# Performance work log

Hardware: AMD Instinct MI355X
Metric: run time of the kernel (lower is better)

Reference implementation:

```python
import jax, jax.numpy as jnp
import numpy as np

N_QUBITS = 12
R = 1
EDGES = [(i, (i + 1) % N_QUBITS) for i in range(N_QUBITS)]
DIM = 2 ** N_QUBITS
BATCH = 64
_LET = 'abcdefghijklmnopqrstuvwxy'

_I4 = np.eye(4, dtype=np.float32)
_AD = np.fliplr(_I4).copy()                      # antidiagonal (XX imag pattern)
_YP = np.array([[0,0,0,1],[0,0,-1,0],[0,-1,0,0],[1,0,0,0]], dtype=np.float32)  # YY imag pattern
_CNOT = jnp.asarray(np.array([[1,0,0,0],[0,1,0,0],[0,0,0,1],[0,0,1,0]], dtype=np.complex64))
_k = np.arange(DIM)
# z_signs[i, k] = -1 if bit (n-i-1) of k is set, matching the torch buffer
_ZS = jnp.asarray(np.stack([1.0 - 2.0 * ((_k >> (N_QUBITS - i - 1)) & 1) for i in range(N_QUBITS)]).astype(np.float32))  # [n, 2^n]


def _c(r, i):
    return jax.lax.complex(r, i)


def rx_mat(t):
    c, s, z = jnp.cos(t / 2), jnp.sin(t / 2), jnp.zeros_like(t)
    real = jnp.stack([jnp.stack([c, z], -1), jnp.stack([z, c], -1)], -2)
    imag = jnp.stack([jnp.stack([z, -s], -1), jnp.stack([-s, z], -1)], -2)
    return _c(real, imag)


def ry_mat(t):
    c, s = jnp.cos(t / 2), jnp.sin(t / 2)
    real = jnp.stack([jnp.stack([c, -s], -1), jnp.stack([s, c], -1)], -2)
    return _c(real, jnp.zeros_like(real))


def rz_mat(t):
    p, z = t / 2, jnp.zeros_like(t)
    cp, sp = jnp.cos(p), jnp.sin(p)
    real = jnp.stack([jnp.stack([cp, z], -1), jnp.stack([z, cp], -1)], -2)
    imag = jnp.stack([jnp.stack([-sp, z], -1), jnp.stack([z, sp], -1)], -2)
    return _c(real, imag)


def ising_zz(t):
    p = t / 2
    c, s = jnp.cos(p), jnp.sin(p)
    dr = jnp.stack([c, c, c, c], -1)
    di = jnp.stack([-s, s, s, -s], -1)
    i4 = jnp.asarray(_I4)
    return _c(dr[..., :, None] * i4, di[..., :, None] * i4)


def ising_xx(t):
    c, s = jnp.cos(t / 2), jnp.sin(t / 2)
    return _c(c[..., None, None] * jnp.asarray(_I4), -s[..., None, None] * jnp.asarray(_AD))


def ising_yy(t):
    c, s = jnp.cos(t / 2), jnp.sin(t / 2)
    return _c(c[..., None, None] * jnp.asarray(_I4), s[..., None, None] * jnp.asarray(_YP))


def apply_1q(state, gate, q):
    # state [B, 2^n]; gate [2,2] or [B,2,2]; qubit axis sits at stride 2^q (matches torch view)
    B = state.shape[0]
    left, right = 2 ** (N_QUBITS - q - 1), 2 ** q
    s = state.reshape(B, left, 2, right)
    sub = 'bij' if gate.ndim == 3 else 'ij'
    return jnp.einsum(f'{sub},bljr->blir', gate, s).reshape(B, DIM)


def apply_2q(state, gate, q1, q2):
    # state [B, 2^n]; gate [4,4]; qubit index = tensor-axis index from MSB (matches torch permute path)
    if q1 > q2:
        q1, q2 = q2, q1
    B = state.shape[0]
    s = state.reshape((B,) + (2,) * N_QUBITS)
    g = gate.reshape(2, 2, 2, 2)
    ax = list(_LET[:N_QUBITS])
    out = ax.copy()
    u, v = ax[q1], ax[q2]
    out[q1], out[q2] = 'A', 'B'
    spec = f"AB{u}{v},Z{''.join(ax)}->Z{''.join(out)}"
    return jnp.einsum(spec, g, s).reshape(B, DIM)


def _forward(data, encoding_scale, encoding_bias, eta, ew_zz, ew_xx, ew_yy, nb_z, nb_x, nb_y, trainable_rots):
    B, n = data.shape
    # data-encoding gates, cached once per forward: angles [B, n] -> gates [B, n, 2, 2]
    rx_g = rx_mat(encoding_scale[:, 0] * data + encoding_bias[:, 0])
    ry_g = ry_mat(encoding_scale[:, 1] * data + encoding_bias[:, 1])
    rz_g = rz_mat(encoding_scale[:, 2] * data + encoding_bias[:, 2])
    state = jnp.zeros((B, DIM), jnp.complex64).at[:, 0].set(1.0)
    ising_fns = (ising_zz, ising_xx, ising_yy)
    ews = (ew_zz, ew_xx, ew_yy)
    nbs = (nb_z, nb_x, nb_y)
    bias_fns = (rz_mat, rx_mat, ry_mat)
    enc_types = ('full', 'xy', 'yz')
    for r in range(R):
        for b in range(3):  # blocks: ZZ, XX, YY
            bt = enc_types[b]
            # data encoding
            for q in range(n):
                if bt != 'yz':
                    state = apply_1q(state, rx_g[:, q], q)
                state = apply_1q(state, ry_g[:, q], q)
                if bt != 'xy':
                    state = apply_1q(state, rz_g[:, q], q)
            # Ising interaction on each edge
            theta = eta[r, b] * ews[b][r]            # [n_edges]
            egs = ising_fns[b](theta)                # [n_edges, 4, 4]
            for e, (i, j) in enumerate(EDGES):
                state = apply_2q(state, egs[e], i, j)
            # node biases (RZ / RX / RY matching the block)
            bgs = bias_fns[b](nbs[b][r])             # [n, 2, 2]
            for q in range(n):
                state = apply_1q(state, bgs[q], q)
            # trainable rotations rx, ry, rz per qubit
            rots = trainable_rots[r, b]              # [n, 3]
            rxg, ryg, rzg = rx_mat(rots[:, 0]), ry_mat(rots[:, 1]), rz_mat(rots[:, 2])
            for q in range(n):
                state = apply_1q(state, rxg[q], q)
                state = apply_1q(state, ryg[q], q)
                state = apply_1q(state, rzg[q], q)
            # CNOT entangling ring
            for q in range(n):
                state = apply_2q(state, _CNOT, q, (q + 1) % n)
    probs = state.real ** 2 + state.imag ** 2        # [B, 2^n]
    return probs @ _ZS.T                             # Pauli-Z expectations [B, n]


def setup_inputs() -> dict:
    key = jax.random.key(0)
    ks = jax.random.split(key, 12)
    n, E, f = N_QUBITS, len(EDGES), jnp.float32
    return {
        'data': jax.random.uniform(ks[0], (BATCH, n), f),
        'encoding_scale': jnp.pi * jnp.ones((n, 3), f) + 0.1 * jax.random.normal(ks[1], (n, 3), f),
        'encoding_bias': 0.1 * jax.random.normal(ks[2], (n, 3), f),
        'eta': 0.5 * jnp.ones((R, 3), f),
        'ew_zz': jnp.ones((R, E), f) + 0.1 * jax.random.normal(ks[3], (R, E), f),
        'ew_xx': jnp.ones((R, E), f) + 0.1 * jax.random.normal(ks[4], (R, E), f),
        'ew_yy': jnp.ones((R, E), f) + 0.1 * jax.random.normal(ks[5], (R, E), f),
        'nb_z': 0.1 * jax.random.normal(ks[6], (R, n), f),
        'nb_x': 0.1 * jax.random.normal(ks[7], (R, n), f),
        'nb_y': 0.1 * jax.random.normal(ks[8], (R, n), f),
        'trainable_rots': 0.1 * jax.random.normal(ks[9], (R, 3, n, 3), f),
    }


def reference(data, encoding_scale, encoding_bias, eta, ew_zz, ew_xx, ew_yy, nb_z, nb_x, nb_y, trainable_rots):
    return _forward(data, encoding_scale, encoding_bias, eta, ew_zz, ew_xx, ew_yy, nb_z, nb_x, nb_y, trainable_rots)
```

## Files before the change

kernel.cpp:

```cpp
#include <hip/hip_runtime.h>
#include <math.h>

#define NT 512
#define QDIM 4096

typedef float v2f __attribute__((ext_vector_type(2)));
using F2 = float2;

__device__ __forceinline__ v2f mkv(float x, float y) { v2f r; r.x = x; r.y = y; return r; }

__device__ __forceinline__ v2f cfma(v2f m, v2f a, v2f acc) {
    v2f r;
    asm("v_pk_fma_f32 %0, %1, %2, %3 op_sel:[0,0,0] op_sel_hi:[0,1,1]\n\t"
        "v_pk_fma_f32 %0, %1, %2, %0 op_sel:[1,1,0] op_sel_hi:[1,0,1] neg_lo:[1,0,0]"
        : "=&v"(r) : "v"(m), "v"(a), "v"(acc));
    return r;
}
__device__ __forceinline__ v2f cmulp(v2f m, v2f a) {
    v2f r;
    asm("v_pk_mul_f32 %0, %1, %2 op_sel:[0,0] op_sel_hi:[0,1]\n\t"
        "v_pk_fma_f32 %0, %1, %2, %0 op_sel:[1,1,0] op_sel_hi:[1,0,1] neg_lo:[1,0,0]"
        : "=&v"(r) : "v"(m), "v"(a));
    return r;
}

__device__ __forceinline__ F2 cadd(F2 p, F2 q) { return make_float2(p.x + q.x, p.y + q.y); }
__device__ __forceinline__ F2 cmul(F2 p, F2 q) {
    return make_float2(p.x * q.x - p.y * q.y, p.x * q.y + p.y * q.x);
}
struct M2 { F2 a, b, c, d; };
__device__ __forceinline__ M2 mmul(M2 A, M2 B) {
    M2 R;
    R.a = cadd(cmul(A.a, B.a), cmul(A.b, B.c));
    R.b = cadd(cmul(A.a, B.b), cmul(A.b, B.d));
    R.c = cadd(cmul(A.c, B.a), cmul(A.d, B.c));
    R.d = cadd(cmul(A.c, B.b), cmul(A.d, B.d));
    return R;
}
__device__ __forceinline__ M2 mrx(float t) {
    float s, c; sincosf(0.5f * t, &s, &c);
    return { make_float2(c, 0), make_float2(0, -s), make_float2(0, -s), make_float2(c, 0) };
}
__device__ __forceinline__ M2 mry(float t) {
    float s, c; sincosf(0.5f * t, &s, &c);
    return { make_float2(c, 0), make_float2(-s, 0), make_float2(s, 0), make_float2(c, 0) };
}
__device__ __forceinline__ M2 mrz(float t) {
    float s, c; sincosf(0.5f * t, &s, &c);
    return { make_float2(c, -s), make_float2(0, 0), make_float2(0, 0), make_float2(c, s) };
}
#define RSQ2 0.70710678118654752f
__device__ __forceinline__ M2 mH() {
    return { make_float2(RSQ2, 0), make_float2(RSQ2, 0), make_float2(RSQ2, 0), make_float2(-RSQ2, 0) };
}
__device__ __forceinline__ M2 mW() {
    return { make_float2(RSQ2, 0), make_float2(0, RSQ2), make_float2(RSQ2, 0), make_float2(0, -RSQ2) };
}
__device__ __forceinline__ M2 mWd() {
    return { make_float2(RSQ2, 0), make_float2(RSQ2, 0), make_float2(0, -RSQ2), make_float2(0, RSQ2) };
}


template<int Li>
__device__ __forceinline__ int kOf(int t, int j) {
    const int mlo = (1 << (3 * Li)) - 1;
    return (t & mlo) | (j << (3 * Li)) | ((t & ~mlo) << 3);
}
__device__ __forceinline__ int slot0(int k) {
    int j = k & 7, t = k >> 3;
    return j * 512 + (t ^ j);
}

template<int TYPE>
__device__ __forceinline__ void itrip(v2f* amp, int l, v2f* wb) {
#pragma unroll
    for (int j = 0; j < 8; ++j) wb[j * 64 + (l ^ ((9 * j) & 63))] = amp[j];
    asm volatile("" ::: "memory");
#pragma unroll
    for (int j = 0; j < 8; ++j) {
        int jo, lo;
        if (TYPE == 0) { jo = l & 7;        lo = j | (l & 56); }
        else           { jo = (l >> 3) & 7; lo = (l & 7) | (j << 3); }
        amp[j] = wb[jo * 64 + (lo ^ ((9 * jo) & 63))];
    }
}

__device__ __forceinline__ void btrip(v2f* amp, int tid, int l, int wv, v2f* b) {
#pragma unroll
    for (int j = 0; j < 8; ++j) b[j * 512 + (tid ^ j)] = amp[j];
    __syncthreads();
#pragma unroll
    for (int j = 0; j < 8; ++j) amp[j] = b[wv * 512 + ((j * 64 + l) ^ wv)];
}

struct Trio { v2f m[12]; };

__device__ __forceinline__ Trio load_trio(const float4 (*g4)[2]) {
    Trio t;
#pragma unroll
    for (int k = 0; k < 3; ++k) {
        float4 a = g4[k][0], b = g4[k][1];
        t.m[k * 4 + 0] = mkv(a.x, a.y); t.m[k * 4 + 1] = mkv(a.z, a.w);
        t.m[k * 4 + 2] = mkv(b.x, b.y); t.m[k * 4 + 3] = mkv(b.z, b.w);
    }
    return t;
}

template<int JB>
__device__ __forceinline__ void g1_reg(v2f* amp, const v2f* g) {
    const int m = 1 << JB;
    v2f m00 = g[0], m01 = g[1], m10 = g[2], m11 = g[3];
#pragma unroll
    for (int j = 0; j < 8; ++j)
        if (!(j & m)) {
            v2f a = amp[j], b = amp[j | m];
            amp[j]     = cfma(m01, b, cmulp(m00, a));
            amp[j | m] = cfma(m11, b, cmulp(m10, a));
        }
}
__device__ __forceinline__ void apply_trio(v2f* amp, const Trio& t) {
    g1_reg<0>(amp, t.m + 0);  g1_reg<1>(amp, t.m + 4);  g1_reg<2>(amp, t.m + 8);
}

__device__ __forceinline__ void diag_L3(v2f* amp, const float* zh, int tid) {
    float phi0 = 0.f;
#pragma unroll
    for (int e = 3; e <= 10; ++e) {
        int hi = 11 - e, lo = 10 - e;
        phi0 += (((tid >> hi) ^ (tid >> lo)) & 1) ? zh[e] : -zh[e];
    }
    float z0 = zh[0], z1 = zh[1], z2 = zh[2], z11 = zh[11];
    int t8 = (tid >> 8) & 1, t0 = tid & 1;
#pragma unroll
    for (int j = 0; j < 8; ++j) {
        int j0 = j & 1, j1 = (j >> 1) & 1, j2 = (j >> 2) & 1;
        float phi = phi0
            + ((j2 ^ j1) ? z0 : -z0)
            + ((j1 ^ j0) ? z1 : -z1)
            + ((j0 ^ t8) ? z2 : -z2)
            + ((j2 ^ t0) ? z11 : -z11);
        float sp, cp;
        __sincosf(phi, &sp, &cp);
        amp[j] = cmulp(mkv(cp, sp), amp[j]);
    }
}

__device__ __forceinline__ int cnot_src(int k) {
#pragma unroll
    for (int e = 11; e >= 0; --e) {
        int hi = (e < 11) ? 11 - e : 11, lo = (e < 11) ? 10 - e : 0;
        if ((k >> hi) & 1) k ^= (1 << lo);
    }
    return k;
}

__device__ __forceinline__ void cnot_trip(v2f* amp, int tid, const int* kslot, v2f* b) {
#pragma unroll
    for (int j = 0; j < 8; ++j) b[j * 512 + (tid ^ j)] = amp[j];
    __syncthreads();
#pragma unroll
    for (int j = 0; j < 8; ++j) amp[j] = b[kslot[j]];
}

__global__ __launch_bounds__(NT) void qsim_kernel(
    const float* __restrict__ data,
    const float* __restrict__ enc_scale,
    const float* __restrict__ enc_bias,
    const float* __restrict__ eta,
    const float* __restrict__ ew_zz,
    const float* __restrict__ ew_xx,
    const float* __restrict__ ew_yy,
    const float* __restrict__ nb_z,
    const float* __restrict__ nb_x,
    const float* __restrict__ nb_y,
    const float* __restrict__ trots,
    float* __restrict__ out)
{
    __shared__ v2f bbuf[2][QDIM];
    __shared__ v2f ibuf[QDIM];
    __shared__ float4 g1q4[72][2];
    __shared__ float zhalf[3][12];
    __shared__ float red[8][12];

    const int tid = threadIdx.x;
    const int l = tid & 63, wv = tid >> 6;
    const int bat = blockIdx.x;
    v2f* wb = &ibuf[wv * 512];

    if (tid < 36) {
        int b = tid / 12, q = tid % 12;
        float x  = data[bat * 12 + q];
        float ax = enc_scale[q * 3 + 0] * x + enc_bias[q * 3 + 0];
        float ay = enc_scale[q * 3 + 1] * x + enc_bias[q * 3 + 1];
        float az = enc_scale[q * 3 + 2] * x + enc_bias[q * 3 + 2];
        M2 M;
        if (b == 0)      M = mmul(mrz(az), mmul(mry(ay), mrx(ax)));
        else if (b == 1) M = mmul(mH(), mmul(mry(ay), mrx(ax)));
        else             M = mmul(mW(), mmul(mrz(az), mry(ay)));
        g1q4[tid][0] = make_float4(M.a.x, M.a.y, M.b.x, M.b.y);
        g1q4[tid][1] = make_float4(M.c.x, M.c.y, M.d.x, M.d.y);
    } else if (tid < 72) {
        int i = tid - 36, b = i / 12, q = i % 12;
        float nb = (b == 0) ? nb_z[q] : (b == 1) ? nb_x[q] : nb_y[q];
        M2 M0 = (b == 0) ? mrz(nb) : (b == 1) ? mrx(nb) : mry(nb);
        float t0 = trots[(b * 12 + q) * 3 + 0];
        float t1 = trots[(b * 12 + q) * 3 + 1];
        float t2 = trots[(b * 12 + q) * 3 + 2];
        M2 M = mmul(mrz(t2), mmul(mry(t1), mmul(mrx(t0), M0)));
        if (b == 1)      M = mmul(M, mH());
        else if (b == 2) M = mmul(M, mWd());
        g1q4[tid][0] = make_float4(M.a.x, M.a.y, M.b.x, M.b.y);
        g1q4[tid][1] = make_float4(M.c.x, M.c.y, M.d.x, M.d.y);
    } else if (tid < 108) {
        int i = tid - 72, b = i / 12, e = i % 12;
        const float* ew = (b == 0) ? ew_zz : (b == 1) ? ew_xx : ew_yy;
        zhalf[b][e] = 0.5f * eta[b] * ew[e];
    }
    __syncthreads();

    v2f amp[8];
#pragma unroll
    for (int j = 0; j < 8; ++j) amp[j] = mkv(0.f, 0.f);
    if (tid == 0) amp[0].x = 1.f;

    int kslot[8];
#pragma unroll
    for (int j = 0; j < 8; ++j)
        kslot[j] = slot0(cnot_src(kOf<0>(tid, j)));

    int sel = 0;
#define NB (&bbuf[(sel ^= 1) ^ 1][0])

    for (int blk = 0; blk < 3; ++blk) {
        const float4(*Ge)[2] = &g1q4[blk * 12];
        const float4(*Gb)[2] = &g1q4[36 + blk * 12];

        Trio tA = load_trio(Ge + 0);
        Trio tB = load_trio(Ge + 3);
        apply_trio(amp, tA);
        itrip<0>(amp, l, wb);
        tA = load_trio(Ge + 6);
        apply_trio(amp, tB);
        itrip<1>(amp, l, wb);
        tB = load_trio(Ge + 9);
        apply_trio(amp, tA);
        btrip(amp, tid, l, wv, NB);
        tA = load_trio(Gb + 9);
        apply_trio(amp, tB);

        diag_L3(amp, zhalf[blk], tid);

        apply_trio(amp, tA);
        btrip(amp, tid, l, wv, NB);
        tA = load_trio(Gb + 6);
        tB = load_trio(Gb + 3);
        apply_trio(amp, tA);
        itrip<1>(amp, l, wb);
        tA = load_trio(Gb + 0);
        apply_trio(amp, tB);
        itrip<0>(amp, l, wb);
        apply_trio(amp, tA);

        cnot_trip(amp, tid, kslot, NB);
    }

    float pr[8];
#pragma unroll
    for (int j = 0; j < 8; ++j) pr[j] = amp[j].x * amp[j].x + amp[j].y * amp[j].y;
    float psum = 0.f;
#pragma unroll
    for (int j = 0; j < 8; ++j) psum += pr[j];

    float acc[12];
#pragma unroll
    for (int i = 0; i < 9; ++i)
        acc[i] = ((tid >> (8 - i)) & 1) ? -psum : psum;
#pragma unroll
    for (int i = 9; i < 12; ++i) {
        float s = 0.f;
        int bit = 11 - i;
#pragma unroll
        for (int j = 0; j < 8; ++j)
            s += ((j >> bit) & 1) ? -pr[j] : pr[j];
        acc[i] = s;
    }
#pragma unroll
    for (int off = 32; off > 0; off >>= 1)
#pragma unroll
        for (int i = 0; i < 12; ++i)
            acc[i] += __shfl_down(acc[i], off, 64);
    if ((tid & 63) == 0)
#pragma unroll
        for (int i = 0; i < 12; ++i) red[wv][i] = acc[i];
    __syncthreads();
    if (tid < 12) {
        float s = 0.f;
#pragma unroll
        for (int ww = 0; ww < 8; ++ww) s += red[ww][tid];
        out[bat * 12 + tid] = s;
    }
}

extern "C" void kernel_launch(void* const* d_in, const int* in_sizes, int n_in,
                              void* d_out, int out_size, void* d_ws, size_t ws_size,
                              hipStream_t stream) {
    const float* data      = (const float*)d_in[0];
    const float* enc_scale = (const float*)d_in[1];
    const float* enc_bias  = (const float*)d_in[2];
    const float* eta       = (const float*)d_in[3];
    const float* ew_zz     = (const float*)d_in[4];
    const float* ew_xx     = (const float*)d_in[5];
    const float* ew_yy     = (const float*)d_in[6];
    const float* nb_z      = (const float*)d_in[7];
    const float* nb_x      = (const float*)d_in[8];
    const float* nb_y      = (const float*)d_in[9];
    const float* trots     = (const float*)d_in[10];
    float* out = (float*)d_out;

    int batch = out_size / 12;
    qsim_kernel<<<batch, NT, 0, stream>>>(data, enc_scale, enc_bias, eta,
                                          ew_zz, ew_xx, ew_yy,
                                          nb_z, nb_x, nb_y, trots, out);
}
```

Baseline: 94.52 us.

## Replace CNOT block barrier with pairwise wave flags and analytic first-layer product state

The first encoding layer acts on the |0> state, so it is computed directly as a product of per-qubit column entries. This skips four gate trios and their shuffles in block 0. The CNOT-permutation __syncthreads is replaced by a per-wave generation flag in LDS. Each wave spins only on the one partner wave whose data it reads, which relaxes the full-block barrier to a point-to-point dependency. The change risks memory-ordering bugs and WAR hazards on the double buffer, and the spin loop has a guard cap.

```diff
diff --git a/kernel.cpp b/kernel.cpp
--- a/kernel.cpp
+++ b/kernel.cpp
@@ -94,7 +94,6 @@
 }
 
 struct Trio { v2f m[12]; };
-
 __device__ __forceinline__ Trio load_trio(const float4 (*g4)[2]) {
     Trio t;
 #pragma unroll
@@ -154,10 +153,21 @@
     return k;
 }
 
-__device__ __forceinline__ void cnot_trip(v2f* amp, int tid, const int* kslot, v2f* b) {
+__device__ __forceinline__ void cnot_pair(v2f* amp, int tid, int l, int pw, int gen,
+                                          const int* kslot, v2f* b,
+                                          volatile unsigned* wflag, int wv) {
 #pragma unroll
     for (int j = 0; j < 8; ++j) b[j * 512 + (tid ^ j)] = amp[j];
-    __syncthreads();
+    asm volatile("" ::: "memory");
+    __threadfence_block();
+    if (l == 0) wflag[wv] = (unsigned)gen;
+    asm volatile("" ::: "memory");
+    int guard = 0;
+    while (wflag[pw] < (unsigned)gen && guard < (1 << 26)) {
+        ++guard;
+        __builtin_amdgcn_s_sleep(1);
+    }
+    asm volatile("" ::: "memory");
 #pragma unroll
     for (int j = 0; j < 8; ++j) amp[j] = b[kslot[j]];
 }
@@ -181,6 +191,7 @@
     __shared__ float4 g1q4[72][2];
     __shared__ float zhalf[3][12];
     __shared__ float red[8][12];
+    __shared__ unsigned wflag[8];
 
     const int tid = threadIdx.x;
     const int l = tid & 63, wv = tid >> 6;
@@ -216,18 +227,18 @@
         const float* ew = (b == 0) ? ew_zz : (b == 1) ? ew_xx : ew_yy;
         zhalf[b][e] = 0.5f * eta[b] * ew[e];
     }
+    if (tid < 8) wflag[tid] = 0u;
     __syncthreads();
 
-    v2f amp[8];
-#pragma unroll
-    for (int j = 0; j < 8; ++j) amp[j] = mkv(0.f, 0.f);
-    if (tid == 0) amp[0].x = 1.f;
+    const int w0 = wv & 1, w1 = (wv >> 1) & 1, w2 = (wv >> 2) & 1;
+    const int pw = (w0 ^ w1) | ((w1 ^ w2) << 1) | (w2 << 2);
 
     int kslot[8];
 #pragma unroll
     for (int j = 0; j < 8; ++j)
         kslot[j] = slot0(cnot_src(kOf<0>(tid, j)));
 
+    v2f amp[8];
     int sel = 0;
 #define NB (&bbuf[(sel ^= 1) ^ 1][0])
 
@@ -235,33 +246,53 @@
         const float4(*Ge)[2] = &g1q4[blk * 12];
         const float4(*Gb)[2] = &g1q4[36 + blk * 12];
 
-        Trio tA = load_trio(Ge + 0);
-        Trio tB = load_trio(Ge + 3);
-        apply_trio(amp, tA);
-        itrip<0>(amp, l, wb);
-        tA = load_trio(Ge + 6);
+        if (blk == 0) {
+            v2f base = mkv(1.f, 0.f);
+#pragma unroll
+            for (int q = 0; q < 9; ++q) {
+                float4 r0 = Ge[q][0], r1 = Ge[q][1];
+                v2f f = ((tid >> q) & 1) ? mkv(r1.x, r1.y) : mkv(r0.x, r0.y);
+                base = cmulp(base, f);
+            }
+            v2f f9[2], f10[2], f11[2];
+            { float4 r0 = Ge[9][0],  r1 = Ge[9][1];  f9[0]  = mkv(r0.x, r0.y); f9[1]  = mkv(r1.x, r1.y); }
+            { float4 r0 = Ge[10][0], r1 = Ge[10][1]; f10[0] = mkv(r0.x, r0.y); f10[1] = mkv(r1.x, r1.y); }
+            { float4 r0 = Ge[11][0], r1 = Ge[11][1]; f11[0] = mkv(r0.x, r0.y); f11[1] = mkv(r1.x, r1.y); }
+#pragma unroll
+            for (int j = 0; j < 8; ++j) {
+                v2f t = cmulp(f9[j & 1], f10[(j >> 1) & 1]);
+                t = cmulp(t, f11[(j >> 2) & 1]);
+                amp[j] = cmulp(t, base);
+            }
+        } else {
+            Trio tA = load_trio(Ge + 0);
+            apply_trio(amp, tA);
+            itrip<0>(amp, l, wb);
+            tA = load_trio(Ge + 3);
+            apply_trio(amp, tA);
+            itrip<1>(amp, l, wb);
+            tA = load_trio(Ge + 6);
+            apply_trio(amp, tA);
+            btrip(amp, tid, l, wv, NB);
+            tA = load_trio(Ge + 9);
+            apply_trio(amp, tA);
+        }
+
+        diag_L3(amp, zhalf[blk], tid);
+
+        Trio tB = load_trio(Gb + 9);
+        apply_trio(amp, tB);
+        btrip(amp, tid, l, wv, NB);
+        tB = load_trio(Gb + 6);
         apply_trio(amp, tB);
         itrip<1>(amp, l, wb);
-        tB = load_trio(Ge + 9);
-        apply_trio(amp, tA);
-        btrip(amp, tid, l, wv, NB);
-        tA = load_trio(Gb + 9);
-        apply_trio(amp, tB);
-
-        diag_L3(amp, zhalf[blk], tid);
-
-        apply_trio(amp, tA);
-        btrip(amp, tid, l, wv, NB);
-        tA = load_trio(Gb + 6);
         tB = load_trio(Gb + 3);
-        apply_trio(amp, tA);
-        itrip<1>(amp, l, wb);
-        tA = load_trio(Gb + 0);
         apply_trio(amp, tB);
         itrip<0>(amp, l, wb);
-        apply_trio(amp, tA);
-
-        cnot_trip(amp, tid, kslot, NB);
+        tB = load_trio(Gb + 0);
+        apply_trio(amp, tB);
+
+        cnot_pair(amp, tid, l, pw, blk + 1, kslot, NB, wflag, wv);
     }
 
     float pr[8];
@@ -289,7 +320,7 @@
 #pragma unroll
         for (int i = 0; i < 12; ++i)
             acc[i] += __shfl_down(acc[i], off, 64);
-    if ((tid & 63) == 0)
+    if (l == 0)
 #pragma unroll
         for (int i = 0; i < 12; ++i) red[wv][i] = acc[i];
     __syncthreads();
```

Result: faster. 91.30 us, median of 2 (-3.4%).
